# Kernel tuning notes

Measured on AMD Instinct MI355X. Metric: run time of the kernel, lower is better.

The kernel has to match this reference:

```python
import jax, jax.numpy as jnp
import numpy as np

N_NODES = 50000
N_EDGES = 800000
IN_DIM = 128
HID = 64
N_LAYERS = 3


def setup_inputs() -> dict:
    key = jax.random.key(0)
    ks = jax.random.split(key, 12)
    x = jax.random.normal(ks[0], (N_NODES, IN_DIM), dtype=jnp.float32)
    edge_index = jax.random.randint(ks[1], (2, N_EDGES), 0, N_NODES, dtype=jnp.int64)
    s = 0.05
    Wp = jax.random.normal(ks[2], (IN_DIM, HID), dtype=jnp.float32) * s
    bp = jax.random.normal(ks[3], (HID,), dtype=jnp.float32) * s
    # per-layer EdgeConv MLP params, stacked over layers
    W1 = jax.random.normal(ks[4], (N_LAYERS, 2 * HID, HID), dtype=jnp.float32) * s
    b1 = jax.random.normal(ks[5], (N_LAYERS, HID), dtype=jnp.float32) * s
    W2 = jax.random.normal(ks[6], (N_LAYERS, HID, HID), dtype=jnp.float32) * s
    b2 = jax.random.normal(ks[7], (N_LAYERS, HID), dtype=jnp.float32) * s
    Wo = jax.random.normal(ks[8], (HID, 1), dtype=jnp.float32) * s
    bo = jax.random.normal(ks[9], (1,), dtype=jnp.float32) * s
    return {"x": x, "edge_index": edge_index, "Wp": Wp, "bp": bp,
            "W1": W1, "b1": b1, "W2": W2, "b2": b2, "Wo": Wo, "bo": bo}


def _edge_conv(h, src, dst, W1, b1, W2, b2):
    # PyG EdgeConv: message = MLP(cat[x_i, x_j - x_i]), aggr = max over incoming edges
    xi = h[dst]                       # [E, H] center (target) features
    xj = h[src]                       # [E, H] neighbor (source) features
    e = jnp.concatenate([xi, xj - xi], axis=-1)   # [E, 2H]
    m = jnp.maximum(e @ W1 + b1, 0.0) @ W2 + b2   # [E, H]
    agg = jax.ops.segment_max(m, dst, num_segments=N_NODES)  # [N, H]
    # nodes with no incoming edges get 0 (PyG scatter-max fill value)
    return jnp.where(jnp.isfinite(agg), agg, 0.0)


def reference(x, edge_index, Wp, bp, W1, b1, W2, b2, Wo, bo):
    src, dst = edge_index[0], edge_index[1]
    h = x @ Wp + bp                   # input projection [N, H]
    for l in range(N_LAYERS):
        residual = h
        h = _edge_conv(h, src, dst, W1[l], b1[l], W2[l], b2[l])
        h = jnp.maximum(h, 0.0)       # relu; dropout is identity in eval
        h = h + residual
    return (h @ Wo + bo)[:, 0]        # squeeze(-1) -> [N]
```

## Files before the change

kernel.cpp:

```cpp
#include <hip/hip_runtime.h>

#define NN 50000
#define IN_DIM 128
#define HID 64
#define NLAYERS 3
#define NB 1563
#define CH 128
#define NPART 8
#define BPP 196

typedef __attribute__((ext_vector_type(8))) short bf16x8;
typedef __attribute__((ext_vector_type(4))) float f32x4;

__device__ __forceinline__ unsigned f2bf(float f) {
    unsigned u = __float_as_uint(f);
    return (u + 0x7fffu + ((u >> 16) & 1u)) >> 16;
}

__device__ __forceinline__ unsigned pk2bf(float a, float b) {
    return __builtin_amdgcn_perm(__float_as_uint(b) + 0x8000u,
                                 __float_as_uint(a) + 0x8000u, 0x07060302u);
}

__device__ __forceinline__ unsigned pack_r(unsigned q, float pA, float pB) {
    float lo = fmaxf(__uint_as_float(q << 16) + pA, 0.f);
    float hi = fmaxf(__uint_as_float(q & 0xffff0000u) + pB, 0.f);
    return pk2bf(lo, hi);
}


__global__ void __launch_bounds__(256) k_hist(const int* __restrict__ dst,
                                              int* __restrict__ cntc, int E, int CE) {
    __shared__ int lh[NB];
    int g = blockIdx.x;
    for (int i = threadIdx.x; i < NB; i += 256) lh[i] = 0;
    __syncthreads();
    int e0 = g * CE, e1 = min(E, e0 + CE);
    for (int e = e0 + threadIdx.x; e < e1; e += 256) atomicAdd(&lh[dst[e] >> 5], 1);
    __syncthreads();
    for (int i = threadIdx.x; i < NB; i += 256) cntc[g * NB + i] = lh[i];
}

__global__ void k_base(const int* __restrict__ cntc, int* __restrict__ basec,
                       int* __restrict__ bincnt) {
    int b = blockIdx.x * 256 + threadIdx.x;
    if (b < NB) {
        int run = 0;
        for (int g = 0; g < CH; g++) {
            basec[g * NB + b] = run;
            run += cntc[g * NB + b];
        }
        bincnt[b] = run;
    }
}

__global__ void k_binscan(const int* __restrict__ bincnt, int* __restrict__ binoff) {
    __shared__ int s[256];
    int t = threadIdx.x;
    int carry = 0;
    for (int c0 = 0; c0 < NB; c0 += 256) {
        int v = (c0 + t < NB) ? bincnt[c0 + t] : 0;
        s[t] = v;
        __syncthreads();
        for (int d = 1; d < 256; d <<= 1) {
            int a = (t >= d) ? s[t - d] : 0;
            __syncthreads();
            s[t] += a;
            __syncthreads();
        }
        if (c0 + t < NB) binoff[c0 + t] = carry + s[t] - v;
        carry += s[255];
        __syncthreads();
    }
}

__global__ void __launch_bounds__(256) k_scatter(
    const int* __restrict__ src, const int* __restrict__ dst,
    const int* __restrict__ basec, const int* __restrict__ binoff,
    unsigned* __restrict__ bscratch, int E, int CE) {
    __shared__ int cur[BPP];
    int p = blockIdx.x & (NPART - 1);
    int g = blockIdx.x >> 3;
    int blo = p * BPP, bhi = min(NB, blo + BPP);
    for (int i = threadIdx.x; i < bhi - blo; i += 256) {
        int b = blo + i;
        cur[i] = binoff[b] + basec[g * NB + b];
    }
    __syncthreads();
    int e0 = g * CE, e1 = min(E, e0 + CE);
    for (int e = e0 + threadIdx.x; e < e1; e += 256) {
        int d = dst[e];
        int bin = d >> 5;
        if (bin >= blo && bin < bhi) {
            int pos = atomicAdd(&cur[bin - blo], 1);
            bscratch[pos] = ((unsigned)(d & 31) << 16) | (unsigned)src[e];
        }
    }
}

__global__ void __launch_bounds__(256) k_binsort(
    const unsigned* __restrict__ bscratch, const int* __restrict__ bincnt,
    const int* __restrict__ binoff, unsigned short* __restrict__ csr,
    int2* __restrict__ meta) {
    __shared__ unsigned entries[1024];
    __shared__ unsigned short sorted[1024];
    __shared__ int cnt[32];
    int bin = blockIdx.x, t = threadIdx.x;
    int n = bincnt[bin], boff = binoff[bin];
    for (int i = t; i < n; i += 256) entries[i] = bscratch[boff + i];
    if (t < 32) cnt[t] = 0;
    __syncthreads();
    for (int i = t; i < n; i += 256) atomicAdd(&cnt[entries[i] >> 16], 1);
    __syncthreads();
    if (t < 32) {
        int c = cnt[t];
        int s = c;
#pragma unroll
        for (int d = 1; d < 32; d <<= 1) {
            int o = __shfl_up(s, d, 64);
            if (t >= d) s += o;
        }
        int node = bin * 32 + t;
        if (node < NN) meta[node] = make_int2(boff + s - c, c);
        cnt[t] = s - c;
    }
    __syncthreads();
    for (int i = t; i < n; i += 256) {
        unsigned e = entries[i];
        int p = atomicAdd(&cnt[e >> 16], 1);
        sorted[p] = (unsigned short)(e & 0xffffu);
    }
    __syncthreads();
    for (int i = t; i < n; i += 256) csr[boff + i] = sorted[i];
}


__global__ void __launch_bounds__(256) k_projpq(
    const float* __restrict__ x, const float* __restrict__ Wp,
    const float* __restrict__ bp, const float* __restrict__ W1,
    const float* __restrict__ b1, float* __restrict__ h,
    float* __restrict__ P, unsigned short* __restrict__ Qb) {
    __shared__ float hs[4][16][66];
    int lane = threadIdx.x & 63, wave = threadIdx.x >> 6;
    int col = lane & 15, quad = lane >> 4;
    int node0 = (blockIdx.x * 4 + wave) * 16;
    if (node0 >= NN) return;

    bf16x8 bw[4][4];
#pragma unroll
    for (int t = 0; t < 4; t++)
#pragma unroll
        for (int kc = 0; kc < 4; kc++) {
            uint4 u;
#pragma unroll
            for (int jp = 0; jp < 4; jp++) {
                int k0 = kc * 32 + quad * 8 + jp * 2;
                ((unsigned*)&u)[jp] = pk2bf(Wp[k0 * HID + t * 16 + col],
                                            Wp[(k0 + 1) * HID + t * 16 + col]);
            }
            bw[t][kc] = __builtin_bit_cast(bf16x8, u);
        }
    const float4* xr = (const float4*)(x + (size_t)(node0 + col) * IN_DIM);
    bf16x8 ax[4];
#pragma unroll
    for (int kc = 0; kc < 4; kc++) {
        float4 f0 = xr[kc * 8 + quad * 2], f1 = xr[kc * 8 + quad * 2 + 1];
        uint4 u;
        u.x = pk2bf(f0.x, f0.y); u.y = pk2bf(f0.z, f0.w);
        u.z = pk2bf(f1.x, f1.y); u.w = pk2bf(f1.z, f1.w);
        ax[kc] = __builtin_bit_cast(bf16x8, u);
    }
#pragma unroll
    for (int t = 0; t < 4; t++) {
        f32x4 c = (f32x4)(0.f);
#pragma unroll
        for (int kc = 0; kc < 4; kc++)
            c = __builtin_amdgcn_mfma_f32_16x16x32_bf16(ax[kc], bw[t][kc], c, 0, 0, 0);
        float bv = bp[t * 16 + col];
#pragma unroll
        for (int r = 0; r < 4; r++) {
            float hv = c[r] + bv;
            int row = quad * 4 + r;
            h[(size_t)(node0 + row) * HID + t * 16 + col] = hv;
            hs[wave][row][t * 16 + col] = hv;
        }
    }

    bf16x8 bfr[8][2];
#pragma unroll
    for (int t = 0; t < 8; t++)
#pragma unroll
        for (int hf = 0; hf < 2; hf++) {
            uint4 u;
#pragma unroll
            for (int jp = 0; jp < 4; jp++) {
                int k0 = hf * 32 + quad * 8 + jp * 2;
                float w0, w1v;
                if (t < 4) {
                    int n = t * 16 + col;
                    w0  = W1[k0 * HID + n] - W1[(HID + k0) * HID + n];
                    w1v = W1[(k0 + 1) * HID + n] - W1[(HID + k0 + 1) * HID + n];
                } else {
                    int n = (t - 4) * 16 + col;
                    w0  = W1[(HID + k0) * HID + n];
                    w1v = W1[(HID + k0 + 1) * HID + n];
                }
                ((unsigned*)&u)[jp] = pk2bf(w0, w1v);
            }
            bfr[t][hf] = __builtin_bit_cast(bf16x8, u);
        }
    const float* hl = &hs[wave][col][0];
    uint4 au, bu;
    {
        float2 e0 = *(const float2*)(hl + quad * 8);
        float2 e1 = *(const float2*)(hl + quad * 8 + 2);
        float2 e2 = *(const float2*)(hl + quad * 8 + 4);
        float2 e3 = *(const float2*)(hl + quad * 8 + 6);
        au.x = pk2bf(e0.x, e0.y); au.y = pk2bf(e1.x, e1.y);
        au.z = pk2bf(e2.x, e2.y); au.w = pk2bf(e3.x, e3.y);
        float2 f0 = *(const float2*)(hl + 32 + quad * 8);
        float2 f1 = *(const float2*)(hl + 32 + quad * 8 + 2);
        float2 f2 = *(const float2*)(hl + 32 + quad * 8 + 4);
        float2 f3 = *(const float2*)(hl + 32 + quad * 8 + 6);
        bu.x = pk2bf(f0.x, f0.y); bu.y = pk2bf(f1.x, f1.y);
        bu.z = pk2bf(f2.x, f2.y); bu.w = pk2bf(f3.x, f3.y);
    }
    bf16x8 a0 = __builtin_bit_cast(bf16x8, au);
    bf16x8 a1 = __builtin_bit_cast(bf16x8, bu);
#pragma unroll
    for (int t = 0; t < 8; t++) {
        f32x4 c = __builtin_amdgcn_mfma_f32_16x16x32_bf16(a0, bfr[t][0], (f32x4)(0.f), 0, 0, 0);
        c = __builtin_amdgcn_mfma_f32_16x16x32_bf16(a1, bfr[t][1], c, 0, 0, 0);
        if (t < 4) {
            float bv = b1[t * 16 + col];
#pragma unroll
            for (int r = 0; r < 4; r++)
                P[(size_t)(node0 + quad * 4 + r) * HID + t * 16 + col] = c[r] + bv;
        } else {
#pragma unroll
            for (int r = 0; r < 4; r++)
                Qb[(size_t)(node0 + quad * 4 + r) * HID + (t - 4) * 16 + col] =
                    (unsigned short)f2bf(c[r]);
        }
    }
}

__global__ void __launch_bounds__(256) k_pq_mfma(
    const float* __restrict__ h, const float* __restrict__ W1,
    const float* __restrict__ b1, float* __restrict__ P,
    unsigned short* __restrict__ Qb, int layer) {
    int lane = threadIdx.x & 63, wave = threadIdx.x >> 6;
    int col = lane & 15, quad = lane >> 4;
    int node0 = (blockIdx.x * 4 + wave) * 16;
    if (node0 >= NN) return;
    const float* W1l = W1 + layer * 2 * HID * HID;

    bf16x8 bfr[8][2];
#pragma unroll
    for (int t = 0; t < 8; t++)
#pragma unroll
        for (int hf = 0; hf < 2; hf++) {
            uint4 u;
#pragma unroll
            for (int jp = 0; jp < 4; jp++) {
                int k0 = hf * 32 + quad * 8 + jp * 2;
                float w0, w1v;
                if (t < 4) {
                    int n = t * 16 + col;
                    w0  = W1l[k0 * HID + n] - W1l[(HID + k0) * HID + n];
                    w1v = W1l[(k0 + 1) * HID + n] - W1l[(HID + k0 + 1) * HID + n];
                } else {
                    int n = (t - 4) * 16 + col;
                    w0  = W1l[(HID + k0) * HID + n];
                    w1v = W1l[(HID + k0 + 1) * HID + n];
                }
                ((unsigned*)&u)[jp] = pk2bf(w0, w1v);
            }
            bfr[t][hf] = __builtin_bit_cast(bf16x8, u);
        }

    const float* hrow = h + (size_t)(node0 + col) * HID;
    float4 ha0 = *(const float4*)(hrow + quad * 8);
    float4 ha1 = *(const float4*)(hrow + quad * 8 + 4);
    float4 hb0 = *(const float4*)(hrow + 32 + quad * 8);
    float4 hb1 = *(const float4*)(hrow + 32 + quad * 8 + 4);
    uint4 au, bu;
    au.x = pk2bf(ha0.x, ha0.y); au.y = pk2bf(ha0.z, ha0.w);
    au.z = pk2bf(ha1.x, ha1.y); au.w = pk2bf(ha1.z, ha1.w);
    bu.x = pk2bf(hb0.x, hb0.y); bu.y = pk2bf(hb0.z, hb0.w);
    bu.z = pk2bf(hb1.x, hb1.y); bu.w = pk2bf(hb1.z, hb1.w);
    bf16x8 a0 = __builtin_bit_cast(bf16x8, au);
    bf16x8 a1 = __builtin_bit_cast(bf16x8, bu);

#pragma unroll
    for (int t = 0; t < 8; t++) {
        f32x4 c = __builtin_amdgcn_mfma_f32_16x16x32_bf16(a0, bfr[t][0], (f32x4)(0.f), 0, 0, 0);
        c = __builtin_amdgcn_mfma_f32_16x16x32_bf16(a1, bfr[t][1], c, 0, 0, 0);
        if (t < 4) {
            float bv = b1[layer * HID + t * 16 + col];
#pragma unroll
            for (int r = 0; r < 4; r++)
                P[(size_t)(node0 + quad * 4 + r) * HID + t * 16 + col] = c[r] + bv;
        } else {
#pragma unroll
            for (int r = 0; r < 4; r++)
                Qb[(size_t)(node0 + quad * 4 + r) * HID + (t - 4) * 16 + col] =
                    (unsigned short)f2bf(c[r]);
        }
    }
}

__global__ void __launch_bounds__(256) k_edge(
    const float* __restrict__ P, const unsigned short* __restrict__ Qb,
    const float* __restrict__ W2, const float* __restrict__ b2,
    const int2* __restrict__ meta, const unsigned short* __restrict__ csr,
    float* __restrict__ h, int layer, int nw,
    int fin, const float* __restrict__ Wo, const float* __restrict__ bo,
    float* __restrict__ outp) {
    __shared__ uint4 qstage[4][16][9];
    int lane = threadIdx.x & 63;
    int col = lane & 15, quad = lane >> 4;
    int wave = threadIdx.x >> 6;
    int rrow = lane >> 3, sseg = lane & 7;
    int wid = (blockIdx.x * blockDim.x + threadIdx.x) >> 6;

    const float* W2l = W2 + layer * HID * HID;
    bf16x8 bfr[4][2];
#pragma unroll
    for (int t = 0; t < 4; t++)
#pragma unroll
        for (int hf = 0; hf < 2; hf++) {
            uint4 u;
#pragma unroll
            for (int jp = 0; jp < 4; jp++) {
                int k0 = hf * 32 + quad * 8 + jp * 2;
                ((unsigned*)&u)[jp] = pk2bf(W2l[k0 * HID + t * 16 + col],
                                            W2l[(k0 + 1) * HID + t * 16 + col]);
            }
            bfr[t][hf] = __builtin_bit_cast(bf16x8, u);
        }
    float b2v = b2[layer * HID + lane];
    float wov = fin ? Wo[lane] : 0.f;

    for (int node = wid; node < NN; node += nw) {
        int2 md = meta[node];
        int start = __builtin_amdgcn_readfirstlane(md.x);
        int cnt   = __builtin_amdgcn_readfirstlane(md.y);
        float res = h[(size_t)node * HID + lane];
        float outv = 0.f;
        if (cnt > 0) {
            const float4* prow = (const float4*)(P + (size_t)node * HID);
            float4 pA = prow[quad * 2], pB = prow[quad * 2 + 1];
            float4 pC = prow[8 + quad * 2], pD = prow[8 + quad * 2 + 1];
            f32x4 mx[4];
#pragma unroll
            for (int t = 0; t < 4; t++) mx[t] = (f32x4)(-3.4e38f);
            for (int b0 = 0; b0 < cnt; b0 += 16) {
                int e1 = b0 + rrow, e2 = b0 + 8 + rrow;
                int s1 = csr[start + (e1 < cnt ? e1 : b0)];
                int s2 = csr[start + (e2 < cnt ? e2 : b0)];
                uint4 v1 = ((const uint4*)(Qb + (size_t)s1 * HID))[sseg];
                uint4 v2 = ((const uint4*)(Qb + (size_t)s2 * HID))[sseg];
                qstage[wave][rrow][sseg] = v1;
                qstage[wave][8 + rrow][sseg] = v2;
                uint4 q0 = qstage[wave][col][quad];
                uint4 q1 = qstage[wave][col][4 + quad];
                uint4 a0u, a1u;
                a0u.x = pack_r(q0.x, pA.x, pA.y);
                a0u.y = pack_r(q0.y, pA.z, pA.w);
                a0u.z = pack_r(q0.z, pB.x, pB.y);
                a0u.w = pack_r(q0.w, pB.z, pB.w);
                a1u.x = pack_r(q1.x, pC.x, pC.y);
                a1u.y = pack_r(q1.y, pC.z, pC.w);
                a1u.z = pack_r(q1.z, pD.x, pD.y);
                a1u.w = pack_r(q1.w, pD.z, pD.w);
                bf16x8 a0 = __builtin_bit_cast(bf16x8, a0u);
                bf16x8 a1 = __builtin_bit_cast(bf16x8, a1u);
#pragma unroll
                for (int t = 0; t < 4; t++) {
                    f32x4 c = __builtin_amdgcn_mfma_f32_16x16x32_bf16(
                        a0, bfr[t][0], (f32x4)(0.f), 0, 0, 0);
                    c = __builtin_amdgcn_mfma_f32_16x16x32_bf16(
                        a1, bfr[t][1], c, 0, 0, 0);
#pragma unroll
                    for (int r = 0; r < 4; r++)
                        mx[t][r] = fmaxf(mx[t][r], c[r]);
                }
            }
            float v[4];
#pragma unroll
            for (int t = 0; t < 4; t++) {
                v[t] = fmaxf(fmaxf(mx[t][0], mx[t][1]), fmaxf(mx[t][2], mx[t][3]));
                v[t] = fmaxf(v[t], __shfl_xor(v[t], 16, 64));
                v[t] = fmaxf(v[t], __shfl_xor(v[t], 32, 64));
            }
            float vs = quad == 0 ? v[0] : quad == 1 ? v[1] : quad == 2 ? v[2] : v[3];
            outv = fmaxf(vs + b2v, 0.f);
        }
        float hv = outv + res;
        h[(size_t)node * HID + lane] = hv;
        if (fin) {
            float v = hv * wov;
#pragma unroll
            for (int m = 32; m >= 1; m >>= 1) v += __shfl_xor(v, m, 64);
            if (lane == 0) outp[node] = v + bo[0];
        }
    }
}

extern "C" void kernel_launch(void* const* d_in, const int* in_sizes, int n_in,
                              void* d_out, int out_size, void* d_ws, size_t ws_size,
                              hipStream_t stream) {
    const float* x  = (const float*)d_in[0];
    const int*   ei = (const int*)d_in[1];
    const float* Wp = (const float*)d_in[2];
    const float* bp = (const float*)d_in[3];
    const float* W1 = (const float*)d_in[4];
    const float* b1 = (const float*)d_in[5];
    const float* W2 = (const float*)d_in[6];
    const float* b2 = (const float*)d_in[7];
    const float* Wo = (const float*)d_in[8];
    const float* bo = (const float*)d_in[9];
    float* out = (float*)d_out;

    const int E = in_sizes[1] / 2;
    const int N = NN;
    const int* srcp = ei;
    const int* dstp = ei + E;

    float* h  = (float*)d_ws;
    float* Pb = h + (size_t)N * HID;
    unsigned short* Qb = (unsigned short*)(Pb + (size_t)N * HID);
    int* cntc   = (int*)(Qb + (size_t)N * HID);
    int* basec  = cntc + CH * NB;
    int* bincnt = basec + CH * NB;
    int* binoff = bincnt + NB;
    int2* meta  = (int2*)(binoff + NB);
    unsigned* bscratch = (unsigned*)(meta + N);
    unsigned short* csr = (unsigned short*)(bscratch + E);

    const int CE = (E + CH - 1) / CH;

    k_hist<<<CH, 256, 0, stream>>>(dstp, cntc, E, CE);
    k_base<<<(NB + 255) / 256, 256, 0, stream>>>(cntc, basec, bincnt);
    k_binscan<<<1, 256, 0, stream>>>(bincnt, binoff);
    k_scatter<<<CH * NPART, 256, 0, stream>>>(srcp, dstp, basec, binoff, bscratch, E, CE);
    k_binsort<<<NB, 256, 0, stream>>>(bscratch, bincnt, binoff, csr, meta);

    const int PQ_BLOCKS = (N / 16 + 3) / 4;
    k_projpq<<<PQ_BLOCKS, 256, 0, stream>>>(x, Wp, bp, W1, b1, h, Pb, Qb);

    const int EDGE_BLOCKS = 2048;
    const int NW = EDGE_BLOCKS * 256 / 64;
    for (int l = 0; l < NLAYERS; l++) {
        if (l > 0)
            k_pq_mfma<<<PQ_BLOCKS, 256, 0, stream>>>(h, W1, b1, Pb, Qb, l);
        k_edge<<<EDGE_BLOCKS, 256, 0, stream>>>(Pb, Qb, W2, b2, meta, csr, h, l, NW,
                                                l == NLAYERS - 1 ? 1 : 0, Wo, bo, out);
    }
}
```

Baseline: 311.0 us.

## Fuse histogram into projection kernel, store P as bf16, use nontemporal accesses

Merges the dst histogram blocks into the input-projection/PQ kernel so both run in a single launch, with blocks split by index. The P buffer (the per-node center term) is now stored in bf16 instead of fp32, which halves its write and read traffic in the edge kernel. Streaming loads and stores of h, x, P and Q use nontemporal hints. It adds bf16 rounding error on P and changes cache behaviour for h, which is re-read by later layers.

After: 337.9 us. 1.09x slower.

```diff
diff --git a/kernel.cpp b/kernel.cpp
--- a/kernel.cpp
+++ b/kernel.cpp
@@ -8,9 +8,11 @@
 #define CH 128
 #define NPART 8
 #define BPP 196
+#define PQ_BLOCKS 782
 
 typedef __attribute__((ext_vector_type(8))) short bf16x8;
 typedef __attribute__((ext_vector_type(4))) float f32x4;
+typedef __attribute__((ext_vector_type(4))) unsigned int u32x4;
 
 __device__ __forceinline__ unsigned f2bf(float f) {
     unsigned u = __float_as_uint(f);
@@ -22,24 +24,15 @@
                                  __float_as_uint(a) + 0x8000u, 0x07060302u);
 }
 
+__device__ __forceinline__ float bflo(unsigned u) { return __uint_as_float(u << 16); }
+__device__ __forceinline__ float bfhi(unsigned u) { return __uint_as_float(u & 0xffff0000u); }
+
 __device__ __forceinline__ unsigned pack_r(unsigned q, float pA, float pB) {
-    float lo = fmaxf(__uint_as_float(q << 16) + pA, 0.f);
-    float hi = fmaxf(__uint_as_float(q & 0xffff0000u) + pB, 0.f);
+    float lo = fmaxf(bflo(q) + pA, 0.f);
+    float hi = fmaxf(bfhi(q) + pB, 0.f);
     return pk2bf(lo, hi);
 }
 
-
-__global__ void __launch_bounds__(256) k_hist(const int* __restrict__ dst,
-                                              int* __restrict__ cntc, int E, int CE) {
-    __shared__ int lh[NB];
-    int g = blockIdx.x;
-    for (int i = threadIdx.x; i < NB; i += 256) lh[i] = 0;
-    __syncthreads();
-    int e0 = g * CE, e1 = min(E, e0 + CE);
-    for (int e = e0 + threadIdx.x; e < e1; e += 256) atomicAdd(&lh[dst[e] >> 5], 1);
-    __syncthreads();
-    for (int i = threadIdx.x; i < NB; i += 256) cntc[g * NB + i] = lh[i];
-}
 
 __global__ void k_base(const int* __restrict__ cntc, int* __restrict__ basec,
                        int* __restrict__ bincnt) {
@@ -134,13 +127,27 @@
     for (int i = t; i < n; i += 256) csr[boff + i] = sorted[i];
 }
 
-
-__global__ void __launch_bounds__(256) k_projpq(
+__global__ void __launch_bounds__(256) k_front(
     const float* __restrict__ x, const float* __restrict__ Wp,
     const float* __restrict__ bp, const float* __restrict__ W1,
     const float* __restrict__ b1, float* __restrict__ h,
-    float* __restrict__ P, unsigned short* __restrict__ Qb) {
-    __shared__ float hs[4][16][66];
+    unsigned short* __restrict__ P, unsigned short* __restrict__ Qb,
+    const int* __restrict__ dst, int* __restrict__ cntc, int E, int CE) {
+    __shared__ char smraw[4 * 16 * 66 * 4];
+
+    if (blockIdx.x >= PQ_BLOCKS) {
+        int* lh = (int*)smraw;
+        int g = blockIdx.x - PQ_BLOCKS;
+        for (int i = threadIdx.x; i < NB; i += 256) lh[i] = 0;
+        __syncthreads();
+        int e0 = g * CE, e1 = min(E, e0 + CE);
+        for (int e = e0 + threadIdx.x; e < e1; e += 256) atomicAdd(&lh[dst[e] >> 5], 1);
+        __syncthreads();
+        for (int i = threadIdx.x; i < NB; i += 256) cntc[g * NB + i] = lh[i];
+        return;
+    }
+
+    float (*hs)[16][66] = (float (*)[16][66])smraw;
     int lane = threadIdx.x & 63, wave = threadIdx.x >> 6;
     int col = lane & 15, quad = lane >> 4;
     int node0 = (blockIdx.x * 4 + wave) * 16;
@@ -160,11 +167,12 @@
             }
             bw[t][kc] = __builtin_bit_cast(bf16x8, u);
         }
-    const float4* xr = (const float4*)(x + (size_t)(node0 + col) * IN_DIM);
+    const f32x4* xr = (const f32x4*)(x + (size_t)(node0 + col) * IN_DIM);
     bf16x8 ax[4];
 #pragma unroll
     for (int kc = 0; kc < 4; kc++) {
-        float4 f0 = xr[kc * 8 + quad * 2], f1 = xr[kc * 8 + quad * 2 + 1];
+        f32x4 f0 = __builtin_nontemporal_load(&xr[kc * 8 + quad * 2]);
+        f32x4 f1 = __builtin_nontemporal_load(&xr[kc * 8 + quad * 2 + 1]);
         uint4 u;
         u.x = pk2bf(f0.x, f0.y); u.y = pk2bf(f0.z, f0.w);
         u.z = pk2bf(f1.x, f1.y); u.w = pk2bf(f1.z, f1.w);
@@ -181,7 +189,7 @@
         for (int r = 0; r < 4; r++) {
             float hv = c[r] + bv;
             int row = quad * 4 + r;
-            h[(size_t)(node0 + row) * HID + t * 16 + col] = hv;
+            __builtin_nontemporal_store(hv, &h[(size_t)(node0 + row) * HID + t * 16 + col]);
             hs[wave][row][t * 16 + col] = hv;
         }
     }
@@ -235,19 +243,22 @@
             float bv = b1[t * 16 + col];
 #pragma unroll
             for (int r = 0; r < 4; r++)
-                P[(size_t)(node0 + quad * 4 + r) * HID + t * 16 + col] = c[r] + bv;
+                __builtin_nontemporal_store(
+                    (unsigned short)f2bf(c[r] + bv),
+                    &P[(size_t)(node0 + quad * 4 + r) * HID + t * 16 + col]);
         } else {
 #pragma unroll
             for (int r = 0; r < 4; r++)
-                Qb[(size_t)(node0 + quad * 4 + r) * HID + (t - 4) * 16 + col] =
-                    (unsigned short)f2bf(c[r]);
+                __builtin_nontemporal_store(
+                    (unsigned short)f2bf(c[r]),
+                    &Qb[(size_t)(node0 + quad * 4 + r) * HID + (t - 4) * 16 + col]);
         }
     }
 }
 
 __global__ void __launch_bounds__(256) k_pq_mfma(
     const float* __restrict__ h, const float* __restrict__ W1,
-    const float* __restrict__ b1, float* __restrict__ P,
+    const float* __restrict__ b1, unsigned short* __restrict__ P,
     unsigned short* __restrict__ Qb, int layer) {
     int lane = threadIdx.x & 63, wave = threadIdx.x >> 6;
     int col = lane & 15, quad = lane >> 4;
@@ -279,11 +290,11 @@
             bfr[t][hf] = __builtin_bit_cast(bf16x8, u);
         }
 
-    const float* hrow = h + (size_t)(node0 + col) * HID;
-    float4 ha0 = *(const float4*)(hrow + quad * 8);
-    float4 ha1 = *(const float4*)(hrow + quad * 8 + 4);
-    float4 hb0 = *(const float4*)(hrow + 32 + quad * 8);
-    float4 hb1 = *(const float4*)(hrow + 32 + quad * 8 + 4);
+    const f32x4* hrow = (const f32x4*)(h + (size_t)(node0 + col) * HID);
+    f32x4 ha0 = __builtin_nontemporal_load(&hrow[quad * 2]);
+    f32x4 ha1 = __builtin_nontemporal_load(&hrow[quad * 2 + 1]);
+    f32x4 hb0 = __builtin_nontemporal_load(&hrow[8 + quad * 2]);
+    f32x4 hb1 = __builtin_nontemporal_load(&hrow[8 + quad * 2 + 1]);
     uint4 au, bu;
     au.x = pk2bf(ha0.x, ha0.y); au.y = pk2bf(ha0.z, ha0.w);
     au.z = pk2bf(ha1.x, ha1.y); au.w = pk2bf(ha1.z, ha1.w);
@@ -300,18 +311,21 @@
             float bv = b1[layer * HID + t * 16 + col];
 #pragma unroll
             for (int r = 0; r < 4; r++)
-                P[(size_t)(node0 + quad * 4 + r) * HID + t * 16 + col] = c[r] + bv;
+                __builtin_nontemporal_store(
+                    (unsigned short)f2bf(c[r] + bv),
+                    &P[(size_t)(node0 + quad * 4 + r) * HID + t * 16 + col]);
         } else {
 #pragma unroll
             for (int r = 0; r < 4; r++)
-                Qb[(size_t)(node0 + quad * 4 + r) * HID + (t - 4) * 16 + col] =
-                    (unsigned short)f2bf(c[r]);
+                __builtin_nontemporal_store(
+                    (unsigned short)f2bf(c[r]),
+                    &Qb[(size_t)(node0 + quad * 4 + r) * HID + (t - 4) * 16 + col]);
         }
     }
 }
 
 __global__ void __launch_bounds__(256) k_edge(
-    const float* __restrict__ P, const unsigned short* __restrict__ Qb,
+    const unsigned short* __restrict__ P, const unsigned short* __restrict__ Qb,
     const float* __restrict__ W2, const float* __restrict__ b2,
     const int2* __restrict__ meta, const unsigned short* __restrict__ csr,
     float* __restrict__ h, int layer, int nw,
@@ -346,12 +360,17 @@
         int2 md = meta[node];
         int start = __builtin_amdgcn_readfirstlane(md.x);
         int cnt   = __builtin_amdgcn_readfirstlane(md.y);
-        float res = h[(size_t)node * HID + lane];
+        float res = __builtin_nontemporal_load(&h[(size_t)node * HID + lane]);
         float outv = 0.f;
         if (cnt > 0) {
-            const float4* prow = (const float4*)(P + (size_t)node * HID);
-            float4 pA = prow[quad * 2], pB = prow[quad * 2 + 1];
-            float4 pC = prow[8 + quad * 2], pD = prow[8 + quad * 2 + 1];
+            const u32x4* prow = (const u32x4*)(P + (size_t)node * HID);
+            u32x4 pq0 = __builtin_nontemporal_load(&prow[quad]);
+            u32x4 pq1 = __builtin_nontemporal_load(&prow[4 + quad]);
+            float4 pA, pB, pC, pD;
+            pA.x = bflo(pq0.x); pA.y = bfhi(pq0.x); pA.z = bflo(pq0.y); pA.w = bfhi(pq0.y);
+            pB.x = bflo(pq0.z); pB.y = bfhi(pq0.z); pB.z = bflo(pq0.w); pB.w = bfhi(pq0.w);
+            pC.x = bflo(pq1.x); pC.y = bfhi(pq1.x); pC.z = bflo(pq1.y); pC.w = bfhi(pq1.y);
+            pD.x = bflo(pq1.z); pD.y = bfhi(pq1.z); pD.z = bflo(pq1.w); pD.w = bfhi(pq1.w);
             f32x4 mx[4];
 #pragma unroll
             for (int t = 0; t < 4; t++) mx[t] = (f32x4)(-3.4e38f);
@@ -398,7 +417,7 @@
             outv = fmaxf(vs + b2v, 0.f);
         }
         float hv = outv + res;
-        h[(size_t)node * HID + lane] = hv;
+        __builtin_nontemporal_store(hv, &h[(size_t)node * HID + lane]);
         if (fin) {
             float v = hv * wov;
 #pragma unroll
@@ -429,8 +448,8 @@
     const int* dstp = ei + E;
 
     float* h  = (float*)d_ws;
-    float* Pb = h + (size_t)N * HID;
-    unsigned short* Qb = (unsigned short*)(Pb + (size_t)N * HID);
+    unsigned short* Pb = (unsigned short*)(h + (size_t)N * HID);
+    unsigned short* Qb = Pb + (size_t)N * HID;
     int* cntc   = (int*)(Qb + (size_t)N * HID);
     int* basec  = cntc + CH * NB;
     int* bincnt = basec + CH * NB;
@@ -441,14 +460,12 @@
 
     const int CE = (E + CH - 1) / CH;
 
-    k_hist<<<CH, 256, 0, stream>>>(dstp, cntc, E, CE);
+    k_front<<<PQ_BLOCKS + CH, 256, 0, stream>>>(x, Wp, bp, W1, b1, h, Pb, Qb,
+                                                dstp, cntc, E, CE);
     k_base<<<(NB + 255) / 256, 256, 0, stream>>>(cntc, basec, bincnt);
     k_binscan<<<1, 256, 0, stream>>>(bincnt, binoff);
     k_scatter<<<CH * NPART, 256, 0, stream>>>(srcp, dstp, basec, binoff, bscratch, E, CE);
     k_binsort<<<NB, 256, 0, stream>>>(bscratch, bincnt, binoff, csr, meta);
-
-    const int PQ_BLOCKS = (N / 16 + 3) / 4;
-    k_projpq<<<PQ_BLOCKS, 256, 0, stream>>>(x, Wp, bp, W1, b1, h, Pb, Qb);
 
     const int EDGE_BLOCKS = 2048;
     const int NW = EDGE_BLOCKS * 256 / 64;
```
